# Kernel optimization log

Measured on AMD Instinct MI355X. Metric: run time of the kernel, lower is better.

Reference implementation:

```python
import jax, jax.numpy as jnp
import numpy as np

EPS = 1e-6


def _ln(x, gamma, beta):
    # torch LayerNorm variant here: uses unbiased std (ddof=1) and eps added to std
    mean = jnp.mean(x, axis=-1, keepdims=True)
    std = jnp.std(x, axis=-1, keepdims=True, ddof=1)
    return gamma * (x - mean) / (std + EPS) + beta


def setup_inputs() -> dict:
    key = jax.random.key(0)
    ks = jax.random.split(key, 5)
    B, In, H = 8192, 1024, 1024
    x = jax.random.normal(ks[0], (B, In), dtype=jnp.float32)
    h = jax.random.normal(ks[1], (B, H), dtype=jnp.float32)
    c = jax.random.normal(ks[2], (B, H), dtype=jnp.float32)
    w_ih = jax.random.normal(ks[3], (4 * H, In), dtype=jnp.float32) * (1.0 / np.sqrt(In))
    b_ih = jnp.zeros((4 * H,), dtype=jnp.float32)
    w_hh = jax.random.normal(ks[4], (4 * H, H), dtype=jnp.float32) * (1.0 / np.sqrt(H))
    gamma_ifgo = jnp.ones((4, H), dtype=jnp.float32)
    beta_ifgo = jnp.zeros((4, H), dtype=jnp.float32)
    gamma_c = jnp.ones((H,), dtype=jnp.float32)
    beta_c = jnp.zeros((H,), dtype=jnp.float32)
    return {"x": x, "h": h, "c": c, "w_ih": w_ih, "b_ih": b_ih, "w_hh": w_hh,
            "gamma_ifgo": gamma_ifgo, "beta_ifgo": beta_ifgo,
            "gamma_c": gamma_c, "beta_c": beta_c}


def reference(x, h, c, w_ih, b_ih, w_hh, gamma_ifgo, beta_ifgo, gamma_c, beta_c):
    B = x.shape[0]
    H = c.shape[1]
    # two GEMMs: [B,4H]
    v = jnp.einsum('bi,ki->bk', x, w_ih) + b_ih + jnp.einsum('bh,kh->bk', h, w_hh)
    gates = v.reshape(B, 4, H)  # stacked i, f, g, o (chunk order == stack order)
    gates = _ln(gates, gamma_ifgo, beta_ifgo)  # ParallelLayerNorm over last dim
    i, f, g, o = gates[:, 0], gates[:, 1], gates[:, 2], gates[:, 3]
    f = f + 1.0
    new_c = c * jax.nn.sigmoid(f) + jax.nn.sigmoid(i) * jnp.tanh(g)
    new_c = _ln(new_c, gamma_c, beta_c)
    new_h = jnp.tanh(new_c) * jax.nn.sigmoid(o)
    return new_h, new_c
```

## Files before the change

### kernel.cpp

```cpp
#include <hip/hip_runtime.h>
#include <hip/hip_bf16.h>
#include <cstdint>

typedef __bf16 bf16x8 __attribute__((ext_vector_type(8)));
typedef float  f32x4  __attribute__((ext_vector_type(4)));

#define BDIM 8192
#define KDIM 2048
#define NDIM 4096
#define HDIM 1024
#define LN_EPS 1e-6f
#define NT    (KDIM / 64)
#define TOTA  ((long)BDIM * KDIM)
#define TOTB  ((long)NDIM * KDIM)

__global__ __launch_bounds__(256) void cvt_all_kernel(
    const float* __restrict__ x, const float* __restrict__ h,
    const float* __restrict__ wih, const float* __restrict__ whh,
    __bf16* __restrict__ Abf, __bf16* __restrict__ Bbf)
{
    long e = ((long)blockIdx.x * blockDim.x + threadIdx.x) * 8;
    const float* p0; const float* p1; __bf16* dst; long eo;
    if (e < TOTA) { p0 = x;   p1 = h;   dst = Abf; eo = e; }
    else          { p0 = wih; p1 = whh; dst = Bbf; eo = e - TOTA; }
    long row = eo >> 11;
    long kk  = eo & 2047;
    const float* src = (kk < 1024) ? (p0 + row * 1024 + kk)
                                   : (p1 + row * 1024 + (kk - 1024));
    float4 a = *(const float4*)(src);
    float4 b = *(const float4*)(src + 4);
    bf16x8 o;
    o[0] = (__bf16)a.x; o[1] = (__bf16)a.y; o[2] = (__bf16)a.z; o[3] = (__bf16)a.w;
    o[4] = (__bf16)b.x; o[5] = (__bf16)b.y; o[6] = (__bf16)b.z; o[7] = (__bf16)b.w;
    *(bf16x8*)(dst + eo) = o;
}

__device__ inline void gload_lds16(const void* g, void* l) {
    __builtin_amdgcn_global_load_lds(
        (const __attribute__((address_space(1))) void*)g,
        (__attribute__((address_space(3))) void*)l, 16, 0, 0);
}

#define WAIT_VM(n) asm volatile("s_waitcnt vmcnt(" #n ")" ::: "memory")
#define BARRIER()  __builtin_amdgcn_s_barrier()

template<int Q>
__device__ inline void mma_q(f32x4 (&acc)[8][4],
                             const bf16x8 (&a)[2][2], const bf16x8 (&b)[4][2])
{
#pragma unroll
    for (int ks = 0; ks < 2; ++ks)
#pragma unroll
        for (int u = 0; u < 2; ++u)
#pragma unroll
            for (int nf = 0; nf < 4; ++nf)
                acc[2 * Q + u][nf] = __builtin_amdgcn_mfma_f32_16x16x32_bf16(
                    a[u][ks], b[nf][ks], acc[2 * Q + u][nf], 0, 0, 0);
}

__global__ __launch_bounds__(512, 2) void gemm_8phase_kernel(
    const __bf16* __restrict__ A, const __bf16* __restrict__ Bt,
    const float* __restrict__ bias, __bf16* __restrict__ V)
{
    __shared__ __bf16 smem[2][32768];

    const int tid = threadIdx.x;
    const int l   = tid & 63;
    const int w   = tid >> 6;
    const int wm  = w >> 2;
    const int wn  = w & 3;
    const int lane16 = l & 15;
    const int q16    = l >> 4;

    const int bid = blockIdx.x;
    const int swz = (bid & 7) * 64 + (bid >> 3);
    const int tileN = (swz & 15) * 256;
    const int tileM = (swz >> 4) * 256;

    const int srow  = (w >> 2) * 128 + (w & 3) * 8 + (l >> 3);
    const int sgran = (l & 7) ^ (l >> 3);
    const __bf16* Asrc = A  + (long)(tileM + srow) * KDIM + sgran * 8;
    const __bf16* Bsrc = Bt + (long)(tileN + srow) * KDIM + sgran * 8;
    const int a_dst = (w >> 2) * 8192 + (w & 3) * 512;
    const int b_dst = 16384 + a_dst;

    const int g0os = ((q16 ^ (l & 7))) * 8;
    const int g1os = (((q16 + 4) ^ (l & 7))) * 8;
    const int a_rd = wm * 8192 + lane16 * 64;
    const int b_rd = 16384 + wn * 4096 + lane16 * 64;

    f32x4 acc[8][4] = {};
    bf16x8 aX[2][2], aY[2][2], bP[4][2], bQ[4][2];

    auto stageA = [&](int c, int kt, int p) {
        gload_lds16(Asrc + (long)kt * 64 + (long)p * (32 * KDIM),
                    &smem[c][a_dst + p * 2048]);
    };
    auto stageB = [&](int c, int kt, int p) {
        gload_lds16(Bsrc + (long)kt * 64 + (long)p * (32 * KDIM),
                    &smem[c][b_dst + p * 2048]);
    };
    auto readA = [&](bf16x8 (&d)[2][2], int c, int q) {
        const __bf16* base = &smem[c][a_rd + q * 2048];
#pragma unroll
        for (int u = 0; u < 2; ++u) {
            d[u][0] = *(const bf16x8*)(base + u * 1024 + g0os);
            d[u][1] = *(const bf16x8*)(base + u * 1024 + g1os);
        }
    };
    auto readB = [&](bf16x8 (&d)[4][2], int c) {
        const __bf16* base = &smem[c][b_rd];
#pragma unroll
        for (int nf = 0; nf < 4; ++nf) {
            d[nf][0] = *(const bf16x8*)(base + nf * 1024 + g0os);
            d[nf][1] = *(const bf16x8*)(base + nf * 1024 + g1os);
        }
    };

#pragma unroll
    for (int p = 0; p < 4; ++p) { stageA(0, 0, p); stageB(0, 0, p); }
#pragma unroll
    for (int p = 0; p < 4; ++p) { stageA(1, 1, p); stageB(1, 1, p); }
    WAIT_VM(8);
    BARRIER();
    readB(bP, 0);
    readA(aX, 0, 0);
    asm volatile("s_waitcnt lgkmcnt(0)" ::: "memory");
    BARRIER();

#pragma unroll 1
    for (int i = 0; i < NT / 2; ++i) {
        const int k0 = 2 * i;
        const int k1 = 2 * i + 1;
        const bool st = (i < NT / 2 - 1);

        readA(aY, 0, 1);
        if (st) { stageA(0, k0 + 2, 0); stageB(0, k0 + 2, 0); }
        BARRIER();
        __builtin_amdgcn_s_setprio(1); mma_q<0>(acc, aX, bP); __builtin_amdgcn_s_setprio(0);

        readA(aX, 0, 2);
        if (st) { stageA(0, k0 + 2, 1); stageB(0, k0 + 2, 1); }
        BARRIER();
        __builtin_amdgcn_s_setprio(1); mma_q<1>(acc, aY, bP); __builtin_amdgcn_s_setprio(0);

        readA(aY, 0, 3);
        if (st) { stageA(0, k0 + 2, 2); stageB(0, k0 + 2, 2); }
        BARRIER();
        __builtin_amdgcn_s_setprio(1); mma_q<2>(acc, aX, bP); __builtin_amdgcn_s_setprio(0);

        if (st) { WAIT_VM(6); } else { WAIT_VM(0); }
        readB(bQ, 1);
        readA(aX, 1, 0);
        if (st) { stageA(0, k0 + 2, 3); stageB(0, k0 + 2, 3); }
        BARRIER();
        __builtin_amdgcn_s_setprio(1); mma_q<3>(acc, aY, bP); __builtin_amdgcn_s_setprio(0);

        readA(aY, 1, 1);
        if (st) { stageA(1, k1 + 2, 0); stageB(1, k1 + 2, 0); }
        BARRIER();
        __builtin_amdgcn_s_setprio(1); mma_q<0>(acc, aX, bQ); __builtin_amdgcn_s_setprio(0);

        readA(aX, 1, 2);
        if (st) { stageA(1, k1 + 2, 1); stageB(1, k1 + 2, 1); }
        BARRIER();
        __builtin_amdgcn_s_setprio(1); mma_q<1>(acc, aY, bQ); __builtin_amdgcn_s_setprio(0);

        readA(aY, 1, 3);
        if (st) { stageA(1, k1 + 2, 2); stageB(1, k1 + 2, 2); }
        BARRIER();
        __builtin_amdgcn_s_setprio(1); mma_q<2>(acc, aX, bQ); __builtin_amdgcn_s_setprio(0);

        if (st) {
            WAIT_VM(6);
            readB(bP, 0);
            readA(aX, 0, 0);
            stageA(1, k1 + 2, 3); stageB(1, k1 + 2, 3);
        }
        BARRIER();
        __builtin_amdgcn_s_setprio(1); mma_q<3>(acc, aY, bQ); __builtin_amdgcn_s_setprio(0);
    }

#pragma unroll
    for (int mi = 0; mi < 8; ++mi) {
        const int row = tileM + wm * 128 + mi * 16 + q16 * 4;
#pragma unroll
        for (int ni = 0; ni < 4; ++ni) {
            const int col = tileN + wn * 64 + ni * 16 + lane16;
            const float bv = bias[col];
#pragma unroll
            for (int j = 0; j < 4; ++j)
                V[(long)(row + j) * NDIM + col] = (__bf16)(acc[mi][ni][j] + bv);
        }
    }
}

__device__ inline float sigm_(float x) { return 1.f / (1.f + __expf(-x)); }
__device__ inline float tanh_(float x) { float e = __expf(2.f * x); return 1.f - 2.f / (e + 1.f); }

__global__ __launch_bounds__(256) void ln_lstm_kernel(
    const __bf16* __restrict__ v, const float* __restrict__ cin,
    const float* __restrict__ gamma4, const float* __restrict__ beta4,
    const float* __restrict__ gammac, const float* __restrict__ betac,
    float* __restrict__ out_h, float* __restrict__ out_c)
{
    __shared__ float gbuf[4][1024];
    __shared__ float red[8];

    const int b = blockIdx.x;
    const int t = threadIdx.x;
    const int w = t >> 6;
    const int l = t & 63;

    const __bf16* vb = v + (long)b * 4096 + w * 1024 + l * 16;
    bf16x8 v0 = *(const bf16x8*)(vb);
    bf16x8 v1 = *(const bf16x8*)(vb + 8);
    float xs[16];
#pragma unroll
    for (int q = 0; q < 8; ++q) { xs[q] = (float)v0[q]; xs[8 + q] = (float)v1[q]; }

    float s = 0.f, sq = 0.f;
#pragma unroll
    for (int q = 0; q < 16; ++q) { s += xs[q]; sq += xs[q] * xs[q]; }
#pragma unroll
    for (int m = 32; m >= 1; m >>= 1) { s += __shfl_xor(s, m); sq += __shfl_xor(sq, m); }

    const float mean = s * (1.f / 1024.f);
    const float var  = (sq - s * mean) * (1.f / 1023.f);
    const float invd = 1.f / (sqrtf(var) + LN_EPS);

#pragma unroll
    for (int q = 0; q < 16; ++q) {
        const int idx = l * 16 + q;
        gbuf[w][idx] = gamma4[w * 1024 + idx] * (xs[q] - mean) * invd + beta4[w * 1024 + idx];
    }
    __syncthreads();

    const int j0 = t * 4;
    float4 iv = *(const float4*)&gbuf[0][j0];
    float4 fv = *(const float4*)&gbuf[1][j0];
    float4 gv = *(const float4*)&gbuf[2][j0];
    float4 ov = *(const float4*)&gbuf[3][j0];
    float4 cv = *(const float4*)(cin + (long)b * 1024 + j0);

    float nc[4], oo[4];
    {
        const float ia[4] = {iv.x, iv.y, iv.z, iv.w};
        const float fa[4] = {fv.x, fv.y, fv.z, fv.w};
        const float ga[4] = {gv.x, gv.y, gv.z, gv.w};
        const float oa[4] = {ov.x, ov.y, ov.z, ov.w};
        const float ca[4] = {cv.x, cv.y, cv.z, cv.w};
#pragma unroll
        for (int q = 0; q < 4; ++q) {
            nc[q] = ca[q] * sigm_(fa[q] + 1.f) + sigm_(ia[q]) * tanh_(ga[q]);
            oo[q] = oa[q];
        }
    }

    float s2 = 0.f, sq2 = 0.f;
#pragma unroll
    for (int q = 0; q < 4; ++q) { s2 += nc[q]; sq2 += nc[q] * nc[q]; }
#pragma unroll
    for (int m = 32; m >= 1; m >>= 1) { s2 += __shfl_xor(s2, m); sq2 += __shfl_xor(sq2, m); }
    if (l == 0) { red[w] = s2; red[4 + w] = sq2; }
    __syncthreads();
    const float S  = red[0] + red[1] + red[2] + red[3];
    const float SQ = red[4] + red[5] + red[6] + red[7];
    const float mean2 = S * (1.f / 1024.f);
    const float var2  = (SQ - S * mean2) * (1.f / 1023.f);
    const float invd2 = 1.f / (sqrtf(var2) + LN_EPS);

    float4 hout, cout;
    float ho[4], co[4];
#pragma unroll
    for (int q = 0; q < 4; ++q) {
        const int j = j0 + q;
        const float ncl = gammac[j] * (nc[q] - mean2) * invd2 + betac[j];
        co[q] = ncl;
        ho[q] = tanh_(ncl) * sigm_(oo[q]);
    }
    hout.x = ho[0]; hout.y = ho[1]; hout.z = ho[2]; hout.w = ho[3];
    cout.x = co[0]; cout.y = co[1]; cout.z = co[2]; cout.w = co[3];
    *(float4*)(out_h + (long)b * 1024 + j0) = hout;
    *(float4*)(out_c + (long)b * 1024 + j0) = cout;
}

extern "C" void kernel_launch(void* const* d_in, const int* in_sizes, int n_in,
                              void* d_out, int out_size, void* d_ws, size_t ws_size,
                              hipStream_t stream)
{
    const float* x      = (const float*)d_in[0];
    const float* h      = (const float*)d_in[1];
    const float* c      = (const float*)d_in[2];
    const float* w_ih   = (const float*)d_in[3];
    const float* b_ih   = (const float*)d_in[4];
    const float* w_hh   = (const float*)d_in[5];
    const float* gamma4 = (const float*)d_in[6];
    const float* beta4  = (const float*)d_in[7];
    const float* gammac = (const float*)d_in[8];
    const float* betac  = (const float*)d_in[9];

    char* ws = (char*)d_ws;
    const size_t szA = (size_t)BDIM * KDIM * 2;
    const size_t szB = (size_t)NDIM * KDIM * 2;
    const size_t szV = (size_t)BDIM * NDIM * 2;
    if (ws_size < szA + szB + szV) return;

    __bf16* Abf = (__bf16*)ws;
    __bf16* Bbf = (__bf16*)(ws + szA);
    __bf16* v   = (__bf16*)(ws + szA + szB);

    float* out_h = (float*)d_out;
    float* out_c = out_h + (size_t)BDIM * HDIM;

    cvt_all_kernel<<<dim3((unsigned)((TOTA + TOTB) / 8 / 256)), dim3(256), 0, stream>>>(
        x, h, w_ih, w_hh, Abf, Bbf);

    gemm_8phase_kernel<<<dim3((BDIM / 256) * (NDIM / 256)), dim3(512), 0, stream>>>(
        Abf, Bbf, b_ih, v);

    ln_lstm_kernel<<<dim3(BDIM), dim3(256), 0, stream>>>(
        v, c, gamma4, beta4, gammac, betac, out_h, out_c);
}
```

Measured before the change: 198.1 us.

## Reorder GEMM staging to load B tile first and split B LDS reads

Reorders the global-to-LDS staging within each k-step so the B tile is staged before A, and splits the B fragment reads from LDS into two halves spread across earlier sub-steps with adjusted vmcnt waits. The goal is to smooth LDS read traffic and shorten the stall at the buffer switch where a full B read was previously issued at once. This adds finer-grained wait counts, which risks correctness if the counts do not match outstanding loads, and may add barrier pressure.

```diff
diff --git a/kernel.cpp b/kernel.cpp
--- a/kernel.cpp
+++ b/kernel.cpp
@@ -108,7 +108,7 @@
             d[u][1] = *(const bf16x8*)(base + u * 1024 + g1os);
         }
     };
-    auto readB = [&](bf16x8 (&d)[4][2], int c) {
+    auto readBfull = [&](bf16x8 (&d)[4][2], int c) {
         const __bf16* base = &smem[c][b_rd];
 #pragma unroll
         for (int nf = 0; nf < 4; ++nf) {
@@ -116,14 +116,27 @@
             d[nf][1] = *(const bf16x8*)(base + nf * 1024 + g1os);
         }
     };
-
-#pragma unroll
-    for (int p = 0; p < 4; ++p) { stageA(0, 0, p); stageB(0, 0, p); }
-#pragma unroll
-    for (int p = 0; p < 4; ++p) { stageA(1, 1, p); stageB(1, 1, p); }
+    auto readBh = [&](bf16x8 (&d)[4][2], int c, int hhalf) {
+        const __bf16* base = &smem[c][b_rd];
+#pragma unroll
+        for (int k = 0; k < 2; ++k) {
+            const int nf = 2 * hhalf + k;
+            d[nf][0] = *(const bf16x8*)(base + nf * 1024 + g0os);
+            d[nf][1] = *(const bf16x8*)(base + nf * 1024 + g1os);
+        }
+    };
+
+#pragma unroll
+    for (int p = 0; p < 4; ++p) stageB(0, 0, p);
+#pragma unroll
+    for (int p = 0; p < 4; ++p) stageA(0, 0, p);
+#pragma unroll
+    for (int p = 0; p < 4; ++p) stageB(1, 1, p);
+#pragma unroll
+    for (int p = 0; p < 4; ++p) stageA(1, 1, p);
     WAIT_VM(8);
     BARRIER();
-    readB(bP, 0);
+    readBfull(bP, 0);
     readA(aX, 0, 0);
     asm volatile("s_waitcnt lgkmcnt(0)" ::: "memory");
     BARRIER();
@@ -135,47 +148,51 @@
         const bool st = (i < NT / 2 - 1);
 
         readA(aY, 0, 1);
-        if (st) { stageA(0, k0 + 2, 0); stageB(0, k0 + 2, 0); }
+        if (st) { stageB(0, k0 + 2, 0); stageB(0, k0 + 2, 1); }
         BARRIER();
         __builtin_amdgcn_s_setprio(1); mma_q<0>(acc, aX, bP); __builtin_amdgcn_s_setprio(0);
 
+        if (st) { WAIT_VM(6); } else { WAIT_VM(4); }
         readA(aX, 0, 2);
-        if (st) { stageA(0, k0 + 2, 1); stageB(0, k0 + 2, 1); }
+        readBh(bQ, 1, 0);
+        if (st) { stageB(0, k0 + 2, 2); stageB(0, k0 + 2, 3); }
         BARRIER();
         __builtin_amdgcn_s_setprio(1); mma_q<1>(acc, aY, bP); __builtin_amdgcn_s_setprio(0);
 
         readA(aY, 0, 3);
-        if (st) { stageA(0, k0 + 2, 2); stageB(0, k0 + 2, 2); }
+        readBh(bQ, 1, 1);
+        if (st) { stageA(0, k0 + 2, 0); stageA(0, k0 + 2, 1); }
         BARRIER();
         __builtin_amdgcn_s_setprio(1); mma_q<2>(acc, aX, bP); __builtin_amdgcn_s_setprio(0);
 
+        if (st) { WAIT_VM(8); } else { WAIT_VM(2); }
+        readA(aX, 1, 0);
+        if (st) { stageA(0, k0 + 2, 2); stageA(0, k0 + 2, 3); }
+        BARRIER();
+        __builtin_amdgcn_s_setprio(1); mma_q<3>(acc, aY, bP); __builtin_amdgcn_s_setprio(0);
+
+        readA(aY, 1, 1);
+        if (st) { stageB(1, k1 + 2, 0); stageB(1, k1 + 2, 1); }
+        BARRIER();
+        __builtin_amdgcn_s_setprio(1); mma_q<0>(acc, aX, bQ); __builtin_amdgcn_s_setprio(0);
+
         if (st) { WAIT_VM(6); } else { WAIT_VM(0); }
-        readB(bQ, 1);
-        readA(aX, 1, 0);
-        if (st) { stageA(0, k0 + 2, 3); stageB(0, k0 + 2, 3); }
-        BARRIER();
-        __builtin_amdgcn_s_setprio(1); mma_q<3>(acc, aY, bP); __builtin_amdgcn_s_setprio(0);
-
-        readA(aY, 1, 1);
-        if (st) { stageA(1, k1 + 2, 0); stageB(1, k1 + 2, 0); }
-        BARRIER();
-        __builtin_amdgcn_s_setprio(1); mma_q<0>(acc, aX, bQ); __builtin_amdgcn_s_setprio(0);
-
         readA(aX, 1, 2);
-        if (st) { stageA(1, k1 + 2, 1); stageB(1, k1 + 2, 1); }
+        if (st) readBh(bP, 0, 0);
+        if (st) { stageB(1, k1 + 2, 2); stageB(1, k1 + 2, 3); }
         BARRIER();
         __builtin_amdgcn_s_setprio(1); mma_q<1>(acc, aY, bQ); __builtin_amdgcn_s_setprio(0);
 
         readA(aY, 1, 3);
-        if (st) { stageA(1, k1 + 2, 2); stageB(1, k1 + 2, 2); }
+        if (st) readBh(bP, 0, 1);
+        if (st) { stageA(1, k1 + 2, 0); stageA(1, k1 + 2, 1); }
         BARRIER();
         __builtin_amdgcn_s_setprio(1); mma_q<2>(acc, aX, bQ); __builtin_amdgcn_s_setprio(0);
 
         if (st) {
-            WAIT_VM(6);
-            readB(bP, 0);
+            WAIT_VM(8);
             readA(aX, 0, 0);
-            stageA(1, k1 + 2, 3); stageB(1, k1 + 2, 3);
+            stageA(1, k1 + 2, 2); stageA(1, k1 + 2, 3);
         }
         BARRIER();
         __builtin_amdgcn_s_setprio(1); mma_q<3>(acc, aY, bQ); __builtin_amdgcn_s_setprio(0);
```

Result: no change. 198.4 us (+0.1%).
